# Performance work log

Measured on AMD Instinct MI355X. Metric: run time of the kernel, lower is better.

## Reference

```python
import jax, jax.numpy as jnp
import numpy as np

NEG = -1e10


def setup_inputs() -> dict:
    key = jax.random.key(0)
    ks = jax.random.split(key, 16)
    B, ql, TN, al = 16, 32, 10, 10
    V, E, H = 50000, 300, 256
    inp = {
        'q': jax.random.randint(ks[0], (B, ql), 0, V),
        'alia': jax.random.randint(ks[1], (B, TN, al), 0, V),
        'els': jax.random.uniform(ks[2], (B, TN), jnp.float32),
        'elo': jax.random.uniform(ks[3], (B, TN), jnp.float32),
        'cate': jax.random.uniform(ks[4], (B, TN, 2), jnp.float32),
        # learned params
        'emb': jax.random.normal(ks[5], (V, E), jnp.float32),
        'sim_w': jax.random.normal(ks[6], (3 * E, 1), jnp.float32) * 0.02,
        'sim_b': jnp.zeros((1,), jnp.float32),
        'enc_w': jax.random.normal(ks[7], (2 * E, H), jnp.float32) * 0.02,
        'enc_b': jnp.zeros((H,), jnp.float32),
        'qlin_w': jax.random.normal(ks[8], (H, 1), jnp.float32) * 0.02,
        'qlin_b': jnp.zeros((1,), jnp.float32),
        'cls_w': jax.random.normal(ks[9], (5, 1), jnp.float32) * 0.1,
        'cls_b': jnp.zeros((1,), jnp.float32),
    }
    return inp


def reference(q, alia, els, elo, cate, emb, sim_w, sim_b, enc_w, enc_b,
              qlin_w, qlin_b, cls_w, cls_b):
    B, ql = q.shape
    _, TN, al = alia.shape
    E = emb.shape[1]

    # per-forward L2 renormalization of the embedding table, padding row zeroed
    emb_n = emb / jnp.maximum(jnp.linalg.norm(emb, axis=1, keepdims=True), 1e-12)
    emb_n = emb_n.at[0].set(0.0)

    q_emb = emb_n[q]                       # [B, ql, E]
    a_emb = emb_n[alia].reshape(B, TN * al, E)  # [B, TN*al, E]

    q_mask = (q != 0).astype(jnp.float32)                    # [B, ql]
    a_mask = (alia != 0).reshape(B, TN * al).astype(jnp.float32)
    mask = a_mask[:, :, None] * q_mask[:, None, :]           # [B, TN*al, ql]

    # similar([w, v, w*v]) decomposed: w@W1 + v@W2 + (w*v)@W3 + b (same math,
    # avoids materializing the [B,TN*al,ql,3E] concat)
    W1, W2, W3 = sim_w[:E, 0], sim_w[E:2 * E, 0], sim_w[2 * E:, 0]
    atten = (a_emb @ W1)[:, :, None] + (q_emb @ W2)[:, None, :] \
        + jnp.einsum('bme,bqe->bmq', a_emb * W3, q_emb) + sim_b[0]
    atten = mask * atten + (1.0 - mask) * NEG                # [B, TN*al, ql]
    atten4 = atten.reshape(B, TN, al, ql)

    atten1 = jax.nn.softmax(atten4, axis=3).reshape(B, TN * al, ql)
    alig = jnp.einsum('bmq,bqe->bme', atten1, q_emb)          # [B, TN*al, E]

    enc_in = jnp.concatenate([alig, a_emb], axis=-1)          # [B, TN*al, 2E]
    enc = jax.nn.relu(enc_in @ enc_w + enc_b).reshape(B, TN, al, -1)
    compare = enc.sum(axis=2)                                 # [B, TN, H]
    alia_score = compare @ qlin_w + qlin_b                    # [B, TN, 1]

    feats = jnp.concatenate(
        [elo[:, :, None], els[:, :, None], cate, alia_score], axis=2)  # [B,TN,5]
    logits = (feats @ cls_w + cls_b)[:, :, 0]                 # [B, TN]

    tmask = ((els + elo) != 0).astype(jnp.float32)            # [B, TN]
    mask_logits = tmask * logits + (1.0 - tmask) * NEG

    max_atten = jax.lax.stop_gradient(atten4.max(axis=2))     # [B, TN, ql]
    p = jax.nn.softmax(mask_logits, axis=1)[:, :, None]
    atten_out = jax.nn.softmax((p * max_atten).sum(axis=1), axis=1)  # [B, ql]
    return mask_logits, atten_out
```

## Files before the change

kernel.cpp:

```cpp
#include <hip/hip_runtime.h>
#include <math.h>

#define NEGV (-10000000000.0f)

constexpr int B  = 16;
constexpr int QL = 32;
constexpr int TN = 10;
constexpr int AL = 10;
constexpr int E  = 300;
constexpr int H  = 256;
constexpr int M  = TN * AL;
constexpr int NQ = B * QL;
constexpr int NA = B * M;
constexpr int SQS = 304;

constexpr size_t OFF_AEMB = 0;
constexpr size_t OFF_ATT  = OFF_AEMB + (size_t)NA * SQS;
constexpr size_t OFF_P    = OFF_ATT + (size_t)NA * QL;
constexpr size_t OFF_QW   = OFF_P + (size_t)NA * QL;
constexpr size_t OFF_PS   = OFF_QW + (size_t)NQ * H;

__global__ __launch_bounds__(256) void k2_fused(
    const int* __restrict__ q, const int* __restrict__ alia,
    const float* __restrict__ emb,
    const float* __restrict__ sim_w, const float* __restrict__ sim_b,
    const float* __restrict__ enc_w, float* __restrict__ ws) {
  __shared__ float smem[13248];
  int tid = threadIdx.x;
  int wid = tid >> 6, lane = tid & 63;

  if (blockIdx.x < 320) {
    int mh = blockIdx.x & 1, btn = blockIdx.x >> 1;
    int b = btn / TN;
    int bm0 = btn * AL + mh * 5;
    float* sq    = smem;
    float* sa    = smem + 32 * 308;
    float* a3    = smem + 32 * 308 + 5 * 304;
    float* s_qw2 = a3 + 6 * 304;
    float* s_aw1 = s_qw2 + 32;
    float* s_scA = s_aw1 + 8;

    for (int i = tid; i < 32 * 75; i += 256) {
      int r = i / 75, e4 = i % 75;
      int idx = q[b * QL + r];
      *(float4*)&sq[r * 308 + e4 * 4] =
          *(const float4*)&emb[(size_t)idx * E + e4 * 4];
    }
    for (int i = tid; i < 5 * 75; i += 256) {
      int j = i / 75, e4 = i % 75;
      int idx = alia[bm0 + j];
      *(float4*)&sa[j * 304 + e4 * 4] =
          *(const float4*)&emb[(size_t)idx * E + e4 * 4];
    }
    for (int i = tid; i < 304; i += 256) a3[5 * 304 + i] = 0.f;
    __syncthreads();

    for (int r = wid; r < 37; r += 4) {
      bool isa = r >= 32;
      const float* row = isa ? &sa[(r - 32) * 304] : &sq[r * 308];
      const float* W = isa ? sim_w : (sim_w + E);
      float ss = 0.f, dw = 0.f;
      for (int e = lane; e < E; e += 64) {
        float v = row[e];
        ss += v * v;
        dw += v * W[e];
      }
      #pragma unroll
      for (int off = 32; off > 0; off >>= 1) {
        ss += __shfl_xor(ss, off);
        dw += __shfl_xor(dw, off);
      }
      if (lane == 0) {
        int idx = isa ? alia[bm0 + (r - 32)] : q[b * QL + r];
        float scale = (idx == 0) ? 0.f : (1.f / fmaxf(sqrtf(ss), 1e-12f));
        if (isa) { s_scA[r - 32] = scale; s_aw1[r - 32] = dw * scale; }
        else s_qw2[r] = dw * scale;
      }
    }
    __syncthreads();

    const float* w3 = sim_w + 2 * E;
    for (int i = tid; i < 5 * 75; i += 256) {
      int j = i / 75, e4 = i % 75;
      float sc = s_scA[j];
      float4 v = *(const float4*)&sa[j * 304 + e4 * 4];
      float4 wv = *(const float4*)&w3[e4 * 4];
      float4 vn; vn.x = v.x*sc; vn.y = v.y*sc; vn.z = v.z*sc; vn.w = v.w*sc;
      *(float4*)&ws[OFF_AEMB + (size_t)(bm0 + j) * SQS + e4 * 4] = vn;
      float4 a3v; a3v.x = vn.x*wv.x; a3v.y = vn.y*wv.y;
      a3v.z = vn.z*wv.z; a3v.w = vn.w*wv.w;
      *(float4*)&a3[j * 304 + e4 * 4] = a3v;
    }
    __syncthreads();

    if (wid < 3) {
      int g = lane & 31, l = lane >> 5;
      int m = wid * 2 + l;
      float simb = sim_b[0];
      const float* qr = &sq[g * 308];
      const float* ar = &a3[m * 304];
      float acc = 0.f;
      for (int e4 = 0; e4 < 75; ++e4) {
        float4 qv = *(const float4*)&qr[e4 * 4];
        float4 av = *(const float4*)&ar[e4 * 4];
        acc += av.x*qv.x + av.y*qv.y + av.z*qv.z + av.w*qv.w;
      }
      if (m < 5) {
        int bm = bm0 + m;
        float att = s_aw1[m] + s_qw2[g] + acc + simb;
        if (!(alia[bm] != 0 && q[b * QL + g] != 0)) att = NEGV;
        ws[OFF_ATT + (size_t)bm * QL + g] = att;
        float mx = att;
        #pragma unroll
        for (int off = 1; off < 32; off <<= 1) mx = fmaxf(mx, __shfl_xor(mx, off));
        float ex = expf(att - mx);
        float sm = ex;
        #pragma unroll
        for (int off = 1; off < 32; off <<= 1) sm += __shfl_xor(sm, off);
        ws[OFF_P + (size_t)bm * QL + g] = ex / sm;
      }
    }
  } else {
    int rg = blockIdx.x - 320;
    int nh = rg & 1, rgi = rg >> 1;
    int slot0 = rgi * 8;
    float* sQ = smem;
    float* spart = smem + 8 * 304;
    float* s_scB = spart + 8192;

    for (int i = tid; i < 8 * 75; i += 256) {
      int r = i / 75, e4 = i % 75;
      int idx = q[slot0 + r];
      *(float4*)&sQ[r * 304 + e4 * 4] =
          *(const float4*)&emb[(size_t)idx * E + e4 * 4];
    }
    __syncthreads();
    for (int r = wid; r < 8; r += 4) {
      const float* row = &sQ[r * 304];
      float ss = 0.f;
      for (int e = lane; e < E; e += 64) { float v = row[e]; ss += v * v; }
      #pragma unroll
      for (int off = 32; off > 0; off >>= 1) ss += __shfl_xor(ss, off);
      if (lane == 0) {
        int idx = q[slot0 + r];
        s_scB[r] = (idx == 0) ? 0.f : (1.f / fmaxf(sqrtf(ss), 1e-12f));
      }
    }
    __syncthreads();

    int c = tid & 31, kq = tid >> 5;
    int ks = kq * 40;
    int nch = (kq == 7) ? 5 : 10;
    float acc[8][4] = {};
    for (int ch = 0; ch < nch; ++ch) {
      int k = ks + ch * 4;
      float4 a[8];
      #pragma unroll
      for (int j = 0; j < 8; j++) a[j] = *(const float4*)&sQ[j * 304 + k];
      const float* wp = enc_w + (size_t)k * H + nh * 128 + c * 4;
      #pragma unroll
      for (int e = 0; e < 4; e++) {
        float4 wv = *(const float4*)&wp[e * H];
        #pragma unroll
        for (int j = 0; j < 8; j++) {
          float av = (e == 0) ? a[j].x : (e == 1) ? a[j].y
                   : (e == 2) ? a[j].z : a[j].w;
          acc[j][0] += av * wv.x; acc[j][1] += av * wv.y;
          acc[j][2] += av * wv.z; acc[j][3] += av * wv.w;
        }
      }
    }
    #pragma unroll
    for (int j = 0; j < 8; j++) {
      float4 t; t.x = acc[j][0]; t.y = acc[j][1]; t.z = acc[j][2]; t.w = acc[j][3];
      *(float4*)&spart[((kq * 8 + j) * 32 + c) * 4] = t;
    }
    __syncthreads();
    #pragma unroll
    for (int t = 0; t < 4; t++) {
      int o = tid + t * 256;
      int j = o >> 7, colh = o & 127;
      float s = 0.f;
      #pragma unroll
      for (int kk = 0; kk < 8; kk++)
        s += spart[((kk * 8 + j) * 32 + (colh >> 2)) * 4 + (colh & 3)];
      ws[OFF_QW + (size_t)(slot0 + j) * H + nh * 128 + colh] = s * s_scB[j];
    }
  }
}

__global__ __launch_bounds__(256) void k2b_enc(
    const float* __restrict__ enc_w, const float* __restrict__ enc_b,
    const float* __restrict__ qlin_w, float* __restrict__ ws) {
  int blk = blockIdx.x;
  int nh = blk & 1, jh = (blk >> 1) & 1, btn = blk >> 2;
  int b = btn / TN;
  int tid = threadIdx.x;
  int c = tid & 31, kq = tid >> 5;
  int bm0 = btn * AL + jh * 5;

  __shared__ float sA[5 * 304];
  __shared__ float sP[5 * 32];
  __shared__ float spart[8 * 5 * 32 * 4];
  __shared__ float s_red[2];

  const float* ga = ws + OFF_AEMB + (size_t)bm0 * SQS;
  for (int i = tid; i < 5 * 75; i += 256) {
    int j = i / 75, e4 = i % 75;
    *(float4*)&sA[j * 304 + e4 * 4] = *(const float4*)&ga[j * SQS + e4 * 4];
  }
  if (tid < 160) sP[tid] = ws[OFF_P + (size_t)bm0 * QL + tid];
  __syncthreads();

  float acc[5][4] = {};

  {
    float4 pv[5];
    #pragma unroll
    for (int j = 0; j < 5; j++) pv[j] = *(const float4*)&sP[j * 32 + kq * 4];
    const float* qwb = ws + OFF_QW + (size_t)(b * QL + kq * 4) * H + nh * 128 + c * 4;
    #pragma unroll
    for (int pp = 0; pp < 4; pp++) {
      float4 wv = *(const float4*)&qwb[pp * H];
      #pragma unroll
      for (int j = 0; j < 5; j++) {
        float p = (pp == 0) ? pv[j].x : (pp == 1) ? pv[j].y
                : (pp == 2) ? pv[j].z : pv[j].w;
        acc[j][0] += p * wv.x; acc[j][1] += p * wv.y;
        acc[j][2] += p * wv.z; acc[j][3] += p * wv.w;
      }
    }
  }

  int ks = kq * 40;
  int nch = (kq == 7) ? 5 : 10;
  for (int ch = 0; ch < nch; ++ch) {
    int k = ks + ch * 4;
    float4 a[5];
    #pragma unroll
    for (int j = 0; j < 5; j++) a[j] = *(const float4*)&sA[j * 304 + k];
    const float* wp = enc_w + (size_t)(E + k) * H + nh * 128 + c * 4;
    #pragma unroll
    for (int e = 0; e < 4; e++) {
      float4 wv = *(const float4*)&wp[e * H];
      #pragma unroll
      for (int j = 0; j < 5; j++) {
        float av = (e == 0) ? a[j].x : (e == 1) ? a[j].y
                 : (e == 2) ? a[j].z : a[j].w;
        acc[j][0] += av * wv.x; acc[j][1] += av * wv.y;
        acc[j][2] += av * wv.z; acc[j][3] += av * wv.w;
      }
    }
  }

  #pragma unroll
  for (int j = 0; j < 5; j++) {
    float4 t; t.x = acc[j][0]; t.y = acc[j][1]; t.z = acc[j][2]; t.w = acc[j][3];
    *(float4*)&spart[((kq * 5 + j) * 32 + c) * 4] = t;
  }
  __syncthreads();

  float v = 0.f;
  if (tid < 128) {
    int colh = tid, col = nh * 128 + colh;
    float bias = enc_b[col];
    float s = 0.f;
    #pragma unroll
    for (int j = 0; j < 5; j++) {
      float t = bias;
      #pragma unroll
      for (int kk = 0; kk < 8; kk++)
        t += spart[((kk * 5 + j) * 32 + (colh >> 2)) * 4 + (colh & 3)];
      s += fmaxf(t, 0.f);
    }
    v = s * qlin_w[col];
  }
  #pragma unroll
  for (int off = 32; off > 0; off >>= 1) v += __shfl_down(v, off);
  if (tid < 128 && (tid & 63) == 0) s_red[tid >> 6] = v;
  __syncthreads();
  if (tid == 0) ws[OFF_PS + blk] = s_red[0] + s_red[1];
}

__global__ __launch_bounds__(256) void k3_final(
    const float* __restrict__ els, const float* __restrict__ elo,
    const float* __restrict__ cate, const float* __restrict__ qlin_b,
    const float* __restrict__ cls_w, const float* __restrict__ cls_b,
    const float* __restrict__ ws, float* __restrict__ out) {
  int b = blockIdx.x;
  int tid = threadIdx.x;
  __shared__ float s_logit[TN], s_p[TN];
  __shared__ float s_at[M * QL];

  const float* attb = ws + OFF_ATT + (size_t)b * M * QL;
  for (int i = tid; i < 800; i += 256)
    *(float4*)&s_at[i * 4] = *(const float4*)&attb[i * 4];

  if (tid < TN) {
    const float* ps = ws + OFF_PS + (size_t)(b * TN + tid) * 4;
    float score = ps[0] + ps[1] + ps[2] + ps[3] + qlin_b[0];
    float lo = elo[b * TN + tid], ls = els[b * TN + tid];
    float c0 = cate[(b * TN + tid) * 2 + 0];
    float c1 = cate[(b * TN + tid) * 2 + 1];
    float logit = lo * cls_w[0] + ls * cls_w[1] + c0 * cls_w[2] +
                  c1 * cls_w[3] + score * cls_w[4] + cls_b[0];
    s_logit[tid] = ((ls + lo) != 0.0f) ? logit : NEGV;
  }
  __syncthreads();

  if (tid == 0) {
    float mx = -INFINITY;
    for (int t = 0; t < TN; t++) mx = fmaxf(mx, s_logit[t]);
    float sm = 0.f;
    for (int t = 0; t < TN; t++) sm += expf(s_logit[t] - mx);
    for (int t = 0; t < TN; t++) s_p[t] = expf(s_logit[t] - mx) / sm;
  }
  if (tid < TN) out[b * TN + tid] = s_logit[tid];
  __syncthreads();

  if (tid < QL) {
    float sacc = 0.f;
    for (int tn2 = 0; tn2 < TN; tn2++) {
      float mxa = -INFINITY;
      #pragma unroll
      for (int al = 0; al < AL; al++) {
        mxa = fmaxf(mxa, s_at[(tn2 * AL + al) * QL + tid]);
      }
      sacc += s_p[tn2] * mxa;
    }
    float mx = sacc;
    #pragma unroll
    for (int off = 16; off > 0; off >>= 1) mx = fmaxf(mx, __shfl_xor(mx, off, 32));
    float ex = expf(sacc - mx);
    float sm = ex;
    #pragma unroll
    for (int off = 16; off > 0; off >>= 1) sm += __shfl_xor(sm, off, 32);
    out[B * TN + b * QL + tid] = ex / sm;
  }
}

extern "C" void kernel_launch(void* const* d_in, const int* in_sizes, int n_in,
                              void* d_out, int out_size, void* d_ws, size_t ws_size,
                              hipStream_t stream) {
  const int*   q      = (const int*)  d_in[0];
  const int*   alia   = (const int*)  d_in[1];
  const float* els    = (const float*)d_in[2];
  const float* elo    = (const float*)d_in[3];
  const float* cate   = (const float*)d_in[4];
  const float* emb    = (const float*)d_in[5];
  const float* sim_w  = (const float*)d_in[6];
  const float* sim_b  = (const float*)d_in[7];
  const float* enc_w  = (const float*)d_in[8];
  const float* enc_b  = (const float*)d_in[9];
  const float* qlin_w = (const float*)d_in[10];
  const float* qlin_b = (const float*)d_in[11];
  const float* cls_w  = (const float*)d_in[12];
  const float* cls_b  = (const float*)d_in[13];
  float* out = (float*)d_out;
  float* ws  = (float*)d_ws;

  k2_fused<<<320 + 128, 256, 0, stream>>>(q, alia, emb, sim_w, sim_b, enc_w, ws);
  k2b_enc<<<B * TN * 4, 256, 0, stream>>>(enc_w, enc_b, qlin_w, ws);
  k3_final<<<B, 256, 0, stream>>>(els, elo, cate, qlin_b, cls_w, cls_b, ws, out);
}
```

Before: 34.67 us.

## Overlap norm computation with attention dot, pre-reduce partials via cross-lane shuffles

In the attention blocks, the w3 product is applied to raw embeddings while they load. Three waves then compute the q·a3 dot products while the fourth wave computes the row norms and W1/W2 projections, with normalization applied afterwards as a scalar factor. This removes two barriers and overlaps the two phases, but it serialises all 37 norm rows onto one wave. In both matmul-style paths, partial sums from paired k-groups are combined with a cross-lane shuffle before the shared-memory store, which halves the partial buffer and the final reduction loop.

Measured after the change: 52.24 us. 1.51x slower.

```diff
diff --git a/kernel.cpp b/kernel.cpp
--- a/kernel.cpp
+++ b/kernel.cpp
@@ -25,7 +25,7 @@
     const float* __restrict__ emb,
     const float* __restrict__ sim_w, const float* __restrict__ sim_b,
     const float* __restrict__ enc_w, float* __restrict__ ws) {
-  __shared__ float smem[13248];
+  __shared__ float smem[12992];
   int tid = threadIdx.x;
   int wid = tid >> 6, lane = tid & 63;
 
@@ -35,11 +35,13 @@
     int bm0 = btn * AL + mh * 5;
     float* sq    = smem;
     float* sa    = smem + 32 * 308;
-    float* a3    = smem + 32 * 308 + 5 * 304;
-    float* s_qw2 = a3 + 6 * 304;
-    float* s_aw1 = s_qw2 + 32;
+    float* sa3   = sa + 5 * 304;
+    float* s_qw2 = sa3 + 5 * 304;
+    float* s_scQ = s_qw2 + 32;
+    float* s_aw1 = s_scQ + 32;
     float* s_scA = s_aw1 + 8;
 
+    const float* w3 = sim_w + 2 * E;
     for (int i = tid; i < 32 * 75; i += 256) {
       int r = i / 75, e4 = i % 75;
       int idx = q[b * QL + r];
@@ -49,76 +51,71 @@
     for (int i = tid; i < 5 * 75; i += 256) {
       int j = i / 75, e4 = i % 75;
       int idx = alia[bm0 + j];
-      *(float4*)&sa[j * 304 + e4 * 4] =
-          *(const float4*)&emb[(size_t)idx * E + e4 * 4];
-    }
-    for (int i = tid; i < 304; i += 256) a3[5 * 304 + i] = 0.f;
-    __syncthreads();
-
-    for (int r = wid; r < 37; r += 4) {
-      bool isa = r >= 32;
-      const float* row = isa ? &sa[(r - 32) * 304] : &sq[r * 308];
-      const float* W = isa ? sim_w : (sim_w + E);
-      float ss = 0.f, dw = 0.f;
-      for (int e = lane; e < E; e += 64) {
-        float v = row[e];
-        ss += v * v;
-        dw += v * W[e];
-      }
-      #pragma unroll
-      for (int off = 32; off > 0; off >>= 1) {
-        ss += __shfl_xor(ss, off);
-        dw += __shfl_xor(dw, off);
-      }
-      if (lane == 0) {
-        int idx = isa ? alia[bm0 + (r - 32)] : q[b * QL + r];
-        float scale = (idx == 0) ? 0.f : (1.f / fmaxf(sqrtf(ss), 1e-12f));
-        if (isa) { s_scA[r - 32] = scale; s_aw1[r - 32] = dw * scale; }
-        else s_qw2[r] = dw * scale;
-      }
-    }
-    __syncthreads();
-
-    const float* w3 = sim_w + 2 * E;
+      float4 v = *(const float4*)&emb[(size_t)idx * E + e4 * 4];
+      float4 wv = *(const float4*)&w3[e4 * 4];
+      *(float4*)&sa[j * 304 + e4 * 4] = v;
+      float4 t; t.x = v.x*wv.x; t.y = v.y*wv.y; t.z = v.z*wv.z; t.w = v.w*wv.w;
+      *(float4*)&sa3[j * 304 + e4 * 4] = t;
+    }
+    __syncthreads();
+
+    int g = lane & 31, l = lane >> 5;
+    int m = wid * 2 + l;
+    float acc = 0.f;
+    if (wid < 3) {
+      const float* qr = &sq[g * 308];
+      const float* ar = &sa3[(m % 5) * 304];
+      for (int e4 = 0; e4 < 75; ++e4) {
+        float4 qv = *(const float4*)&qr[e4 * 4];
+        float4 av = *(const float4*)&ar[e4 * 4];
+        acc += av.x*qv.x + av.y*qv.y + av.z*qv.z + av.w*qv.w;
+      }
+    } else {
+      for (int r = 0; r < 37; ++r) {
+        bool isa = r >= 32;
+        const float* row = isa ? &sa[(r - 32) * 304] : &sq[r * 308];
+        const float* W = isa ? sim_w : (sim_w + E);
+        float ss = 0.f, dw = 0.f;
+        for (int e = lane; e < E; e += 64) {
+          float v = row[e];
+          ss += v * v;
+          dw += v * W[e];
+        }
+        #pragma unroll
+        for (int off = 32; off > 0; off >>= 1) {
+          ss += __shfl_xor(ss, off);
+          dw += __shfl_xor(dw, off);
+        }
+        if (lane == 0) {
+          int idx = isa ? alia[bm0 + (r - 32)] : q[b * QL + r];
+          float scale = (idx == 0) ? 0.f : (1.f / fmaxf(sqrtf(ss), 1e-12f));
+          if (isa) { s_scA[r - 32] = scale; s_aw1[r - 32] = dw * scale; }
+          else     { s_scQ[r] = scale;      s_qw2[r] = dw * scale; }
+        }
+      }
+    }
+    __syncthreads();
+
     for (int i = tid; i < 5 * 75; i += 256) {
       int j = i / 75, e4 = i % 75;
       float sc = s_scA[j];
       float4 v = *(const float4*)&sa[j * 304 + e4 * 4];
-      float4 wv = *(const float4*)&w3[e4 * 4];
       float4 vn; vn.x = v.x*sc; vn.y = v.y*sc; vn.z = v.z*sc; vn.w = v.w*sc;
       *(float4*)&ws[OFF_AEMB + (size_t)(bm0 + j) * SQS + e4 * 4] = vn;
-      float4 a3v; a3v.x = vn.x*wv.x; a3v.y = vn.y*wv.y;
-      a3v.z = vn.z*wv.z; a3v.w = vn.w*wv.w;
-      *(float4*)&a3[j * 304 + e4 * 4] = a3v;
-    }
-    __syncthreads();
-
-    if (wid < 3) {
-      int g = lane & 31, l = lane >> 5;
-      int m = wid * 2 + l;
-      float simb = sim_b[0];
-      const float* qr = &sq[g * 308];
-      const float* ar = &a3[m * 304];
-      float acc = 0.f;
-      for (int e4 = 0; e4 < 75; ++e4) {
-        float4 qv = *(const float4*)&qr[e4 * 4];
-        float4 av = *(const float4*)&ar[e4 * 4];
-        acc += av.x*qv.x + av.y*qv.y + av.z*qv.z + av.w*qv.w;
-      }
-      if (m < 5) {
-        int bm = bm0 + m;
-        float att = s_aw1[m] + s_qw2[g] + acc + simb;
-        if (!(alia[bm] != 0 && q[b * QL + g] != 0)) att = NEGV;
-        ws[OFF_ATT + (size_t)bm * QL + g] = att;
-        float mx = att;
-        #pragma unroll
-        for (int off = 1; off < 32; off <<= 1) mx = fmaxf(mx, __shfl_xor(mx, off));
-        float ex = expf(att - mx);
-        float sm = ex;
-        #pragma unroll
-        for (int off = 1; off < 32; off <<= 1) sm += __shfl_xor(sm, off);
-        ws[OFF_P + (size_t)bm * QL + g] = ex / sm;
-      }
+    }
+    if (wid < 3 && m < 5) {
+      int bm = bm0 + m;
+      float att = s_aw1[m] + s_qw2[g] + acc * s_scA[m] * s_scQ[g] + sim_b[0];
+      if (!(alia[bm] != 0 && q[b * QL + g] != 0)) att = NEGV;
+      ws[OFF_ATT + (size_t)bm * QL + g] = att;
+      float mx = att;
+      #pragma unroll
+      for (int off = 1; off < 32; off <<= 1) mx = fmaxf(mx, __shfl_xor(mx, off));
+      float ex = expf(att - mx);
+      float sm = ex;
+      #pragma unroll
+      for (int off = 1; off < 32; off <<= 1) sm += __shfl_xor(sm, off);
+      ws[OFF_P + (size_t)bm * QL + g] = ex / sm;
     }
   } else {
     int rg = blockIdx.x - 320;
@@ -126,7 +123,7 @@
     int slot0 = rgi * 8;
     float* sQ = smem;
     float* spart = smem + 8 * 304;
-    float* s_scB = spart + 8192;
+    float* s_scB = spart + 4096;
 
     for (int i = tid; i < 8 * 75; i += 256) {
       int r = i / 75, e4 = i % 75;
@@ -171,9 +168,16 @@
       }
     }
     #pragma unroll
-    for (int j = 0; j < 8; j++) {
-      float4 t; t.x = acc[j][0]; t.y = acc[j][1]; t.z = acc[j][2]; t.w = acc[j][3];
-      *(float4*)&spart[((kq * 8 + j) * 32 + c) * 4] = t;
+    for (int j = 0; j < 8; j++)
+      #pragma unroll
+      for (int nc = 0; nc < 4; nc++) acc[j][nc] += __shfl_xor(acc[j][nc], 32);
+    if ((kq & 1) == 0) {
+      int kq2 = kq >> 1;
+      #pragma unroll
+      for (int j = 0; j < 8; j++) {
+        float4 t; t.x = acc[j][0]; t.y = acc[j][1]; t.z = acc[j][2]; t.w = acc[j][3];
+        *(float4*)&spart[((kq2 * 8 + j) * 32 + c) * 4] = t;
+      }
     }
     __syncthreads();
     #pragma unroll
@@ -182,7 +186,7 @@
       int j = o >> 7, colh = o & 127;
       float s = 0.f;
       #pragma unroll
-      for (int kk = 0; kk < 8; kk++)
+      for (int kk = 0; kk < 4; kk++)
         s += spart[((kk * 8 + j) * 32 + (colh >> 2)) * 4 + (colh & 3)];
       ws[OFF_QW + (size_t)(slot0 + j) * H + nh * 128 + colh] = s * s_scB[j];
     }
@@ -201,7 +205,7 @@
 
   __shared__ float sA[5 * 304];
   __shared__ float sP[5 * 32];
-  __shared__ float spart[8 * 5 * 32 * 4];
+  __shared__ float spart[4 * 5 * 32 * 4];
   __shared__ float s_red[2];
 
   const float* ga = ws + OFF_AEMB + (size_t)bm0 * SQS;
@@ -254,9 +258,16 @@
   }
 
   #pragma unroll
-  for (int j = 0; j < 5; j++) {
-    float4 t; t.x = acc[j][0]; t.y = acc[j][1]; t.z = acc[j][2]; t.w = acc[j][3];
-    *(float4*)&spart[((kq * 5 + j) * 32 + c) * 4] = t;
+  for (int j = 0; j < 5; j++)
+    #pragma unroll
+    for (int nc = 0; nc < 4; nc++) acc[j][nc] += __shfl_xor(acc[j][nc], 32);
+  if ((kq & 1) == 0) {
+    int kq2 = kq >> 1;
+    #pragma unroll
+    for (int j = 0; j < 5; j++) {
+      float4 t; t.x = acc[j][0]; t.y = acc[j][1]; t.z = acc[j][2]; t.w = acc[j][3];
+      *(float4*)&spart[((kq2 * 5 + j) * 32 + c) * 4] = t;
+    }
   }
   __syncthreads();
 
@@ -269,7 +280,7 @@
     for (int j = 0; j < 5; j++) {
       float t = bias;
       #pragma unroll
-      for (int kk = 0; kk < 8; kk++)
+      for (int kk = 0; kk < 4; kk++)
         t += spart[((kk * 5 + j) * 32 + (colh >> 2)) * 4 + (colh & 3)];
       s += fmaxf(t, 0.f);
     }
```
